# Performance work log

Hardware: AMD Instinct MI355X
Metric: run time of the kernel (lower is better)

## Reference

```python
import jax, jax.numpy as jnp
import numpy as np

B, V, MF, MT, NP, K, R = 16, 20, 32, 8, 4, 3, 12
D, NOUT = 128, 64


def setup_inputs() -> dict:
    key = jax.random.key(0)
    ks = jax.random.split(key, 8)
    source_embed = jax.random.normal(ks[0], (B, V, MT, MF, D), dtype=jnp.float32)
    rel_index = jax.random.uniform(ks[1], (B, V, MF, MT, NP, K, R), dtype=jnp.float32)
    s = jax.random.normal(ks[2], (B, V, NOUT), dtype=jnp.float32)
    # relation weight matrices; W[0] is fixed all-ones (non-trainable in torch)
    xavier = float(np.sqrt(6.0 / (D + D)) * 1.414)
    W_rel = jax.random.uniform(ks[3], (R, D, D), dtype=jnp.float32, minval=-xavier, maxval=xavier)
    W_rel = W_rel.at[0].set(1.0)
    # attention Linear(hidden_dim + noutfeat, 1): input is cat([s, z_j]) -> first NOUT weights for s
    lim_a = float(1.0 / np.sqrt(D + NOUT))
    attn_w = jax.random.uniform(ks[4], (NOUT + D,), dtype=jnp.float32, minval=-lim_a, maxval=lim_a)
    attn_b = jax.random.uniform(ks[5], (), dtype=jnp.float32, minval=-lim_a, maxval=lim_a)
    # output Linear(hidden_dim, noutfeat)
    lim_o = float(1.0 / np.sqrt(D))
    out_w = jax.random.uniform(ks[6], (D, NOUT), dtype=jnp.float32, minval=-lim_o, maxval=lim_o)
    out_b = jax.random.uniform(ks[7], (NOUT,), dtype=jnp.float32, minval=-lim_o, maxval=lim_o)
    return {"source_embed": source_embed, "rel_index": rel_index, "s": s,
            "W_rel": W_rel, "attn_w": attn_w, "attn_b": attn_b,
            "out_w": out_w, "out_b": out_b}


def reference(source_embed, rel_index, s, W_rel, attn_w, attn_b, out_w, out_b):
    nout = s.shape[-1]
    # torch einsum 'bvtfpdd,bvtfd->bvtfpd' takes the DIAGONAL of the per-edge
    # d x d matrices; prod over K is elementwise, so only diagonals are needed.
    diag = jnp.diagonal(W_rel, axis1=-2, axis2=-1)          # [R, D]
    rels = jnp.einsum('bvftpkr,rd->bvftpkd', rel_index, diag)  # [B,V,MF,MT,NP,K,D]
    Wd = jnp.prod(rels, axis=-2)                             # [B,V,MF,MT,NP,D]
    Wd = jnp.transpose(Wd, (0, 1, 3, 2, 4, 5))               # [B,V,MT,MF,NP,D]
    z_j = Wd * source_embed[..., None, :]                    # [B,V,MT,MF,NP,D]
    # attn logits: Linear(cat([s_rep, z_j])) -> split weight into s / z parts
    logits = (jnp.einsum('bvtfpd,d->bvtfp', z_j, attn_w[nout:])
              + (s @ attn_w[:nout])[:, :, None, None, None] + attn_b)
    a = jax.nn.softmax(logits, axis=-1)                      # softmax over paths
    z = jnp.einsum('bvtfp,bvtfpd->bvtfd', a, z_j)            # [B,V,MT,MF,D]
    out = jax.nn.relu(z @ out_w + out_b)                     # [B,V,MT,MF,NOUT]
    return out.sum(axis=-2).sum(axis=-2)                     # sum feat, then target -> [B,V,NOUT]
```

## Files before the change

### kernel.cpp

```cpp
#include <hip/hip_runtime.h>
#include <hip/hip_bf16.h>

typedef short bf16x8 __attribute__((ext_vector_type(8)));
typedef float f32x4  __attribute__((ext_vector_type(4)));
typedef unsigned short u16;

#define Bc    16
#define Vc    20
#define MFc   32
#define MTc   8
#define NPc   4
#define Kc    3
#define Rc    12
#define Dc    128
#define NOUTc 64

#define TOTAL_UNITS (Bc * Vc * MTc * MFc)
#define XPU 144
#define NBLOCKS 1024
#define UPB 80
#define NBATCH 5

__global__ void setup_tabs(const float* __restrict__ W_rel,
                           const float* __restrict__ out_w,
                           u16* __restrict__ ws) {
    const int i = blockIdx.x * 256 + threadIdx.x;
    if (i < 128 * 32) {
        const int d = i >> 5, r = i & 31;
        const float v = (r < Rc) ? W_rel[(r * Dc + d) * Dc + d] : 0.f;
        union { __hip_bfloat16 h; u16 u; } cv; cv.h = __float2bfloat16(v);
        ws[i] = cv.u;
    } else if (i < 128 * 32 + 64 * 128) {
        const int j = i - 128 * 32;
        const int n = j >> 7, d = j & 127;
        union { __hip_bfloat16 h; u16 u; } cv;
        cv.h = __float2bfloat16(out_w[d * NOUTc + n]);
        ws[i] = cv.u;
    }
}

__global__ __launch_bounds__(256)
void gal_kernel(const float* __restrict__ src,
                const float* __restrict__ rel,
                const u16*   __restrict__ diagB,
                const u16*   __restrict__ Wb,
                const float* __restrict__ attn_w,
                const float* __restrict__ out_b,
                float* __restrict__ out)
{
    __shared__ __align__(16) u16 zp[2][16][520];

    const int tid  = threadIdx.x;
    const int lane = tid & 63;
    const int wv   = tid >> 6;
    const int c    = lane & 15;
    const int g    = lane >> 4;

    const int u_base = blockIdx.x * UPB;
    const int bv0    = u_base >> 8;

    bf16x8 wbf[4];
#pragma unroll
    for (int ks = 0; ks < 4; ++ks)
        wbf[ks] = *(const bf16x8*)(Wb + (wv * 16 + c) * Dc + ks * 32 + g * 8);

    const float LOG2E = 1.4426950408889634f;
    float aw_r[8];
#pragma unroll
    for (int t = 0; t < 8; ++t)
        aw_r[t] = attn_w[NOUTc + t * 16 + c] * LOG2E;
    const float ob = out_b[wv * 16 + c];

    const int pA  = c >> 2, klA = c & 3;
    const int rr  = pA * 3 + (klA < 3 ? klA : 2);
    const int ao0 = rr * Rc + (g & 1) * 8;
    const int ao1 = (g == 0) ? (ao0 + 4) : ao0;
    const bool vlo = (g <= 1);
    const bool vhi = (g == 0);

    const f32x4 zero4 = {0.f, 0.f, 0.f, 0.f};
    float accA = 0.f, accB = 0.f;

    for (int b = 0; b < NBATCH; ++b) {
        const int X   = b & 1;
        const int ub0 = u_base + b * 16;

        for (int j = 0; j < 4; ++j) {
            const int u = ub0 + wv * 4 + j;
            const float* __restrict__ xu = rel + u * XPU;
            const float4 La = *(const float4*)(xu + ao0);
            const float4 Lb = *(const float4*)(xu + ao1);

            const int t8 = u & 7, f5 = (u >> 3) & 31, ubv = u >> 8;
            const float* __restrict__ sp = src + ((ubv * MTc + t8) * MFc + f5) * Dc;
            float sld[8];
#pragma unroll
            for (int t = 0; t < 8; ++t) sld[t] = sp[t * 16 + c];

            union { __hip_bfloat162 h; unsigned int q; } q0, q1, q2, q3;
            q0.h = __float22bfloat162_rn(make_float2(La.x, La.y));
            q1.h = __float22bfloat162_rn(make_float2(La.z, La.w));
            q2.h = __float22bfloat162_rn(make_float2(Lb.x, Lb.y));
            q3.h = __float22bfloat162_rn(make_float2(Lb.z, Lb.w));
            union { bf16x8 v; unsigned int q[4]; } af;
            af.q[0] = vlo ? q0.q : 0u;
            af.q[1] = vlo ? q1.q : 0u;
            af.q[2] = vhi ? q2.q : 0u;
            af.q[3] = vhi ? q3.q : 0u;

            f32x4 pa[8];
#pragma unroll
            for (int t = 0; t < 8; ++t) {
                const bf16x8 bf = *(const bf16x8*)(diagB + (t * 16 + c) * 32 + g * 8);
                pa[t] = __builtin_amdgcn_mfma_f32_16x16x32_bf16(af.v, bf, zero4, 0, 0, 0);
            }

            float w[8], lp = 0.f;
#pragma unroll
            for (int t = 0; t < 8; ++t) {
                w[t] = pa[t][0] * pa[t][1] * pa[t][2];
                lp = fmaf(w[t], sld[t] * aw_r[t], lp);
            }
            lp += __shfl_xor(lp, 1);
            lp += __shfl_xor(lp, 2);
            lp += __shfl_xor(lp, 4);
            lp += __shfl_xor(lp, 8);
            const float lA = lp;
            const float lB = __shfl_xor(lp, 16);
            const float lC = __shfl_xor(lp, 32);
            const float lD = __shfl_xor(lB, 32);

            const float m   = fmaxf(fmaxf(lA, lB), fmaxf(lC, lD));
            const float eS  = exp2f(lA - m);
            const float sum = eS + exp2f(lB - m) + exp2f(lC - m) + exp2f(lD - m);
            const float aS  = eS * __builtin_amdgcn_rcpf(sum);

            u16* zr = &zp[X][wv * 4 + j][g * 128 + c];
#pragma unroll
            for (int t = 0; t < 8; ++t) {
                union { __hip_bfloat16 h; u16 u; } cv;
                cv.h = __float2bfloat16(aS * sld[t] * w[t]);
                zr[t * 16] = cv.u;
            }
        }

        __syncthreads();

        f32x4 ca = zero4, cb = zero4;
#pragma unroll
        for (int p = 0; p < 2; ++p)
#pragma unroll
            for (int ks = 0; ks < 4; ++ks) {
                const bf16x8 az = *(const bf16x8*)(&zp[X][c][p * 128 + ks * 32 + g * 8]);
                ca = __builtin_amdgcn_mfma_f32_16x16x32_bf16(az, wbf[ks], ca, 0, 0, 0);
            }
#pragma unroll
        for (int p = 2; p < 4; ++p)
#pragma unroll
            for (int ks = 0; ks < 4; ++ks) {
                const bf16x8 az = *(const bf16x8*)(&zp[X][c][p * 128 + ks * 32 + g * 8]);
                cb = __builtin_amdgcn_mfma_f32_16x16x32_bf16(az, wbf[ks], cb, 0, 0, 0);
            }

        float su = 0.f;
#pragma unroll
        for (int i = 0; i < 4; ++i)
            su += fmaxf(ca[i] + cb[i] + ob, 0.f);
        if ((ub0 >> 8) == bv0) accA += su; else accB += su;
    }

    accA += __shfl_xor(accA, 16); accA += __shfl_xor(accA, 32);
    accB += __shfl_xor(accB, 16); accB += __shfl_xor(accB, 32);
    if (lane < 16) {
        atomicAdd(&out[bv0 * NOUTc + wv * 16 + lane], accA);
        const int bvL = (u_base + UPB - 1) >> 8;
        if (bvL != bv0) atomicAdd(&out[bvL * NOUTc + wv * 16 + lane], accB);
    }
}

extern "C" void kernel_launch(void* const* d_in, const int* in_sizes, int n_in,
                              void* d_out, int out_size, void* d_ws, size_t ws_size,
                              hipStream_t stream) {
    const float* src    = (const float*)d_in[0];
    const float* rel    = (const float*)d_in[1];
    const float* W_rel  = (const float*)d_in[3];
    const float* attn_w = (const float*)d_in[4];
    const float* out_w  = (const float*)d_in[6];
    const float* out_b  = (const float*)d_in[7];
    float* out  = (float*)d_out;
    u16*   tabs = (u16*)d_ws;

    hipMemsetAsync(out, 0, (size_t)out_size * sizeof(float), stream);
    setup_tabs<<<48, 256, 0, stream>>>(W_rel, out_w, tabs);
    gal_kernel<<<NBLOCKS, 256, 0, stream>>>(src, rel, tabs, tabs + 128 * 32,
                                            attn_w, out_b, out);
}
```

Measured before the change: 48.14 us.

## Reduce paths before output GEMM and hoist diag table loads into registers

The attention-weighted sum over the four paths is now done in registers with cross-lane shuffles before the output projection. Each unit writes a single 128-wide row to shared memory instead of four path rows, which cuts shared-memory traffic and the output MFMA count by a factor of four. The per-edge diagonal table fragments are also loaded once per thread into registers rather than reloaded for every unit. This adds shuffles and register pressure, and only 16 lanes perform the shared-memory stores.

```diff
diff --git a/kernel.cpp b/kernel.cpp
--- a/kernel.cpp
+++ b/kernel.cpp
@@ -20,6 +20,7 @@
 #define NBLOCKS 1024
 #define UPB 80
 #define NBATCH 5
+#define ZLD 136
 
 __global__ void setup_tabs(const float* __restrict__ W_rel,
                            const float* __restrict__ out_w,
@@ -48,7 +49,7 @@
                 const float* __restrict__ out_b,
                 float* __restrict__ out)
 {
-    __shared__ __align__(16) u16 zp[2][16][520];
+    __shared__ __align__(16) u16 zp[2][16][ZLD];
 
     const int tid  = threadIdx.x;
     const int lane = tid & 63;
@@ -59,6 +60,10 @@
     const int u_base = blockIdx.x * UPB;
     const int bv0    = u_base >> 8;
 
+    bf16x8 dgf[8];
+#pragma unroll
+    for (int t = 0; t < 8; ++t)
+        dgf[t] = *(const bf16x8*)(diagB + (t * 16 + c) * 32 + g * 8);
     bf16x8 wbf[4];
 #pragma unroll
     for (int ks = 0; ks < 4; ++ks)
@@ -108,17 +113,12 @@
             af.q[2] = vhi ? q2.q : 0u;
             af.q[3] = vhi ? q3.q : 0u;
 
-            f32x4 pa[8];
-#pragma unroll
-            for (int t = 0; t < 8; ++t) {
-                const bf16x8 bf = *(const bf16x8*)(diagB + (t * 16 + c) * 32 + g * 8);
-                pa[t] = __builtin_amdgcn_mfma_f32_16x16x32_bf16(af.v, bf, zero4, 0, 0, 0);
-            }
-
             float w[8], lp = 0.f;
 #pragma unroll
             for (int t = 0; t < 8; ++t) {
-                w[t] = pa[t][0] * pa[t][1] * pa[t][2];
+                const f32x4 pa =
+                    __builtin_amdgcn_mfma_f32_16x16x32_bf16(af.v, dgf[t], zero4, 0, 0, 0);
+                w[t] = pa[0] * pa[1] * pa[2];
                 lp = fmaf(w[t], sld[t] * aw_r[t], lp);
             }
             lp += __shfl_xor(lp, 1);
@@ -135,37 +135,38 @@
             const float sum = eS + exp2f(lB - m) + exp2f(lC - m) + exp2f(lD - m);
             const float aS  = eS * __builtin_amdgcn_rcpf(sum);
 
-            u16* zr = &zp[X][wv * 4 + j][g * 128 + c];
+            float zb[8];
 #pragma unroll
             for (int t = 0; t < 8; ++t) {
-                union { __hip_bfloat16 h; u16 u; } cv;
-                cv.h = __float2bfloat16(aS * sld[t] * w[t]);
-                zr[t * 16] = cv.u;
+                float v = aS * w[t];
+                v += __shfl_xor(v, 16);
+                v += __shfl_xor(v, 32);
+                zb[t] = v * sld[t];
+            }
+            if (lane < 16) {
+                u16* zr = &zp[X][wv * 4 + j][c];
+#pragma unroll
+                for (int t = 0; t < 8; ++t) {
+                    union { __hip_bfloat16 h; u16 u; } cv;
+                    cv.h = __float2bfloat16(zb[t]);
+                    zr[t * 16] = cv.u;
+                }
             }
         }
 
         __syncthreads();
 
-        f32x4 ca = zero4, cb = zero4;
+        f32x4 ca = zero4;
 #pragma unroll
-        for (int p = 0; p < 2; ++p)
-#pragma unroll
-            for (int ks = 0; ks < 4; ++ks) {
-                const bf16x8 az = *(const bf16x8*)(&zp[X][c][p * 128 + ks * 32 + g * 8]);
-                ca = __builtin_amdgcn_mfma_f32_16x16x32_bf16(az, wbf[ks], ca, 0, 0, 0);
-            }
-#pragma unroll
-        for (int p = 2; p < 4; ++p)
-#pragma unroll
-            for (int ks = 0; ks < 4; ++ks) {
-                const bf16x8 az = *(const bf16x8*)(&zp[X][c][p * 128 + ks * 32 + g * 8]);
-                cb = __builtin_amdgcn_mfma_f32_16x16x32_bf16(az, wbf[ks], cb, 0, 0, 0);
-            }
+        for (int ks = 0; ks < 4; ++ks) {
+            const bf16x8 az = *(const bf16x8*)(&zp[X][c][ks * 32 + g * 8]);
+            ca = __builtin_amdgcn_mfma_f32_16x16x32_bf16(az, wbf[ks], ca, 0, 0, 0);
+        }
 
         float su = 0.f;
 #pragma unroll
         for (int i = 0; i < 4; ++i)
-            su += fmaxf(ca[i] + cb[i] + ob, 0.f);
+            su += fmaxf(ca[i] + ob, 0.f);
         if ((ub0 >> 8) == bv0) accA += su; else accB += su;
     }
 
```

Result: slower. 52.99 us (+10.1%).

## Launch one block per 16 units and hoist diagonal fragments into registers

Applied to the files above, without the earlier changes.

The kernel drops the 5-batch loop per block and instead launches TOTAL_UNITS/16 = 5120 blocks, each handling a single batch of 16 units with one shared buffer and one sync. The diagonal-table MFMA operands are loaded once into registers before the unit loop instead of per unit, and the loop is fully unrolled. This trades per-block setup (weight fragment loads, attn_w loads) and many more atomicAdds (5x) for more parallelism and memory latency hiding across blocks.

```diff
diff --git a/kernel.cpp b/kernel.cpp
--- a/kernel.cpp
+++ b/kernel.cpp
@@ -17,9 +17,9 @@
 
 #define TOTAL_UNITS (Bc * Vc * MTc * MFc)
 #define XPU 144
-#define NBLOCKS 1024
-#define UPB 80
-#define NBATCH 5
+#define UPB 16
+#define NBLOCKS (TOTAL_UNITS / UPB)
+#define ZLD 520
 
 __global__ void setup_tabs(const float* __restrict__ W_rel,
                            const float* __restrict__ out_w,
@@ -48,7 +48,7 @@
                 const float* __restrict__ out_b,
                 float* __restrict__ out)
 {
-    __shared__ __align__(16) u16 zp[2][16][520];
+    __shared__ __align__(16) u16 zp[16][ZLD];
 
     const int tid  = threadIdx.x;
     const int lane = tid & 63;
@@ -59,6 +59,10 @@
     const int u_base = blockIdx.x * UPB;
     const int bv0    = u_base >> 8;
 
+    bf16x8 dgf[8];
+#pragma unroll
+    for (int t = 0; t < 8; ++t)
+        dgf[t] = *(const bf16x8*)(diagB + (t * 16 + c) * 32 + g * 8);
     bf16x8 wbf[4];
 #pragma unroll
     for (int ks = 0; ks < 4; ++ks)
@@ -79,103 +83,92 @@
     const bool vhi = (g == 0);
 
     const f32x4 zero4 = {0.f, 0.f, 0.f, 0.f};
-    float accA = 0.f, accB = 0.f;
 
-    for (int b = 0; b < NBATCH; ++b) {
-        const int X   = b & 1;
-        const int ub0 = u_base + b * 16;
+#pragma unroll
+    for (int j = 0; j < 4; ++j) {
+        const int u = u_base + wv * 4 + j;
+        const float* __restrict__ xu = rel + u * XPU;
+        const float4 La = *(const float4*)(xu + ao0);
+        const float4 Lb = *(const float4*)(xu + ao1);
 
-        for (int j = 0; j < 4; ++j) {
-            const int u = ub0 + wv * 4 + j;
-            const float* __restrict__ xu = rel + u * XPU;
-            const float4 La = *(const float4*)(xu + ao0);
-            const float4 Lb = *(const float4*)(xu + ao1);
+        const int t8 = u & 7, f5 = (u >> 3) & 31;
+        const float* __restrict__ sp = src + ((bv0 * MTc + t8) * MFc + f5) * Dc;
+        float sld[8];
+#pragma unroll
+        for (int t = 0; t < 8; ++t) sld[t] = sp[t * 16 + c];
 
-            const int t8 = u & 7, f5 = (u >> 3) & 31, ubv = u >> 8;
-            const float* __restrict__ sp = src + ((ubv * MTc + t8) * MFc + f5) * Dc;
-            float sld[8];
+        union { __hip_bfloat162 h; unsigned int q; } q0, q1, q2, q3;
+        q0.h = __float22bfloat162_rn(make_float2(La.x, La.y));
+        q1.h = __float22bfloat162_rn(make_float2(La.z, La.w));
+        q2.h = __float22bfloat162_rn(make_float2(Lb.x, Lb.y));
+        q3.h = __float22bfloat162_rn(make_float2(Lb.z, Lb.w));
+        union { bf16x8 v; unsigned int q[4]; } af;
+        af.q[0] = vlo ? q0.q : 0u;
+        af.q[1] = vlo ? q1.q : 0u;
+        af.q[2] = vhi ? q2.q : 0u;
+        af.q[3] = vhi ? q3.q : 0u;
+
+        f32x4 pa[8];
 #pragma unroll
-            for (int t = 0; t < 8; ++t) sld[t] = sp[t * 16 + c];
+        for (int t = 0; t < 8; ++t)
+            pa[t] = __builtin_amdgcn_mfma_f32_16x16x32_bf16(af.v, dgf[t], zero4, 0, 0, 0);
 
-            union { __hip_bfloat162 h; unsigned int q; } q0, q1, q2, q3;
-            q0.h = __float22bfloat162_rn(make_float2(La.x, La.y));
-            q1.h = __float22bfloat162_rn(make_float2(La.z, La.w));
-            q2.h = __float22bfloat162_rn(make_float2(Lb.x, Lb.y));
-            q3.h = __float22bfloat162_rn(make_float2(Lb.z, Lb.w));
-            union { bf16x8 v; unsigned int q[4]; } af;
-            af.q[0] = vlo ? q0.q : 0u;
-            af.q[1] = vlo ? q1.q : 0u;
-            af.q[2] = vhi ? q2.q : 0u;
-            af.q[3] = vhi ? q3.q : 0u;
+        float w[8], lp = 0.f;
+#pragma unroll
+        for (int t = 0; t < 8; ++t) {
+            w[t] = pa[t][0] * pa[t][1] * pa[t][2];
+            lp = fmaf(w[t], sld[t] * aw_r[t], lp);
+        }
+        lp += __shfl_xor(lp, 1);
+        lp += __shfl_xor(lp, 2);
+        lp += __shfl_xor(lp, 4);
+        lp += __shfl_xor(lp, 8);
+        const float lA = lp;
+        const float lB = __shfl_xor(lp, 16);
+        const float lC = __shfl_xor(lp, 32);
+        const float lD = __shfl_xor(lB, 32);
 
-            f32x4 pa[8];
+        const float m   = fmaxf(fmaxf(lA, lB), fmaxf(lC, lD));
+        const float eS  = exp2f(lA - m);
+        const float sum = eS + exp2f(lB - m) + exp2f(lC - m) + exp2f(lD - m);
+        const float aS  = eS * __builtin_amdgcn_rcpf(sum);
+
+        u16* zr = &zp[wv * 4 + j][g * 128 + c];
 #pragma unroll
-            for (int t = 0; t < 8; ++t) {
-                const bf16x8 bf = *(const bf16x8*)(diagB + (t * 16 + c) * 32 + g * 8);
-                pa[t] = __builtin_amdgcn_mfma_f32_16x16x32_bf16(af.v, bf, zero4, 0, 0, 0);
-            }
+        for (int t = 0; t < 8; ++t) {
+            union { __hip_bfloat16 h; u16 u; } cv;
+            cv.h = __float2bfloat16(aS * sld[t] * w[t]);
+            zr[t * 16] = cv.u;
+        }
+    }
 
-            float w[8], lp = 0.f;
+    __syncthreads();
+
+    f32x4 ca = zero4, cb = zero4;
 #pragma unroll
-            for (int t = 0; t < 8; ++t) {
-                w[t] = pa[t][0] * pa[t][1] * pa[t][2];
-                lp = fmaf(w[t], sld[t] * aw_r[t], lp);
-            }
-            lp += __shfl_xor(lp, 1);
-            lp += __shfl_xor(lp, 2);
-            lp += __shfl_xor(lp, 4);
-            lp += __shfl_xor(lp, 8);
-            const float lA = lp;
-            const float lB = __shfl_xor(lp, 16);
-            const float lC = __shfl_xor(lp, 32);
-            const float lD = __shfl_xor(lB, 32);
-
-            const float m   = fmaxf(fmaxf(lA, lB), fmaxf(lC, lD));
-            const float eS  = exp2f(lA - m);
-            const float sum = eS + exp2f(lB - m) + exp2f(lC - m) + exp2f(lD - m);
-            const float aS  = eS * __builtin_amdgcn_rcpf(sum);
-
-            u16* zr = &zp[X][wv * 4 + j][g * 128 + c];
+    for (int p = 0; p < 2; ++p)
 #pragma unroll
-            for (int t = 0; t < 8; ++t) {
-                union { __hip_bfloat16 h; u16 u; } cv;
-                cv.h = __float2bfloat16(aS * sld[t] * w[t]);
-                zr[t * 16] = cv.u;
-            }
+        for (int ks = 0; ks < 4; ++ks) {
+            const bf16x8 az = *(const bf16x8*)(&zp[c][p * 128 + ks * 32 + g * 8]);
+            ca = __builtin_amdgcn_mfma_f32_16x16x32_bf16(az, wbf[ks], ca, 0, 0, 0);
+        }
+#pragma unroll
+    for (int p = 2; p < 4; ++p)
+#pragma unroll
+        for (int ks = 0; ks < 4; ++ks) {
+            const bf16x8 az = *(const bf16x8*)(&zp[c][p * 128 + ks * 32 + g * 8]);
+            cb = __builtin_amdgcn_mfma_f32_16x16x32_bf16(az, wbf[ks], cb, 0, 0, 0);
         }
 
-        __syncthreads();
+    float acc = 0.f;
+#pragma unroll
+    for (int i = 0; i < 4; ++i)
+        acc += fmaxf(ca[i] + cb[i] + ob, 0.f);
 
-        f32x4 ca = zero4, cb = zero4;
-#pragma unroll
-        for (int p = 0; p < 2; ++p)
-#pragma unroll
-            for (int ks = 0; ks < 4; ++ks) {
-                const bf16x8 az = *(const bf16x8*)(&zp[X][c][p * 128 + ks * 32 + g * 8]);
-                ca = __builtin_amdgcn_mfma_f32_16x16x32_bf16(az, wbf[ks], ca, 0, 0, 0);
-            }
-#pragma unroll
-        for (int p = 2; p < 4; ++p)
-#pragma unroll
-            for (int ks = 0; ks < 4; ++ks) {
-                const bf16x8 az = *(const bf16x8*)(&zp[X][c][p * 128 + ks * 32 + g * 8]);
-                cb = __builtin_amdgcn_mfma_f32_16x16x32_bf16(az, wbf[ks], cb, 0, 0, 0);
-            }
-
-        float su = 0.f;
-#pragma unroll
-        for (int i = 0; i < 4; ++i)
-            su += fmaxf(ca[i] + cb[i] + ob, 0.f);
-        if ((ub0 >> 8) == bv0) accA += su; else accB += su;
-    }
-
-    accA += __shfl_xor(accA, 16); accA += __shfl_xor(accA, 32);
-    accB += __shfl_xor(accB, 16); accB += __shfl_xor(accB, 32);
-    if (lane < 16) {
-        atomicAdd(&out[bv0 * NOUTc + wv * 16 + lane], accA);
-        const int bvL = (u_base + UPB - 1) >> 8;
-        if (bvL != bv0) atomicAdd(&out[bvL * NOUTc + wv * 16 + lane], accB);
-    }
+    acc += __shfl_xor(acc, 16);
+    acc += __shfl_xor(acc, 32);
+    if (lane < 16)
+        atomicAdd(&out[bv0 * NOUTc + wv * 16 + lane], acc);
 }
 
 extern "C" void kernel_launch(void* const* d_in, const int* in_sizes, int n_in,
```

After: 53.35 us. 1.11x slower.
